# Kernel optimization log

Measured on AMD Instinct MI355X. Metric: run time of the kernel, lower is better.

## Reference

```python
import jax, jax.numpy as jnp
import numpy as np
from jax import lax

EPS = 1e-5
HEADS = 8

def _proj(x, i, w1, b1, g1, be1, m1, v1, w2, b2, g2, be2, m2, v2):
    # Conv2d(1,8,3,1,1) -> BN(8) -> ReLU -> Conv2d(8,1,3,1,1) -> BN(1) -> ReLU (eval-mode BN)
    dn = ('NCHW', 'OIHW', 'NCHW')
    def bn(y, g, b, m, v):
        return g[None, :, None, None] * (y - m[None, :, None, None]) * lax.rsqrt(v + EPS)[None, :, None, None] + b[None, :, None, None]
    y = lax.conv_general_dilated(x, w1[i], (1, 1), 'SAME', dimension_numbers=dn) + b1[i][None, :, None, None]
    y = jax.nn.relu(bn(y, g1[i], be1[i], m1[i], v1[i]))
    y = lax.conv_general_dilated(y, w2[i], (1, 1), 'SAME', dimension_numbers=dn) + b2[i][None, :, None, None]
    return jax.nn.relu(bn(y, g2[i], be2[i], m2[i], v2[i]))

def setup_inputs() -> dict:
    key = jax.random.key(0)
    ks = jax.random.split(key, 4)
    B, L, D = 4, 512, 512
    X = jax.random.normal(ks[0], (B, L, D), dtype=jnp.float32)
    valid_lens = jax.random.randint(ks[1], (B,), 1, L + 1, dtype=jnp.int32)
    # stacked params for the 4 projection blocks: 0=Q, 1=K, 2=V, 3=out
    w1 = jax.random.normal(ks[2], (4, 8, 1, 3, 3), dtype=jnp.float32) * 0.2
    w2 = jax.random.normal(ks[3], (4, 1, 8, 3, 3), dtype=jnp.float32) * 0.2
    b1 = jnp.zeros((4, 8), jnp.float32); b2 = jnp.zeros((4, 1), jnp.float32)
    g1 = jnp.ones((4, 8), jnp.float32);  g2 = jnp.ones((4, 1), jnp.float32)
    be1 = jnp.zeros((4, 8), jnp.float32); be2 = jnp.zeros((4, 1), jnp.float32)
    m1 = jnp.zeros((4, 8), jnp.float32);  m2 = jnp.zeros((4, 1), jnp.float32)
    v1 = jnp.ones((4, 8), jnp.float32);   v2 = jnp.ones((4, 1), jnp.float32)
    return {"X": X, "valid_lens": valid_lens, "w1": w1, "b1": b1, "g1": g1, "be1": be1,
            "m1": m1, "v1": v1, "w2": w2, "b2": b2, "g2": g2, "be2": be2, "m2": m2, "v2": v2}

def reference(X, valid_lens, w1, b1, g1, be1, m1, v1, w2, b2, g2, be2, m2, v2):
    B, L, D = X.shape
    H = HEADS
    d = D // H
    p = (w1, b1, g1, be1, m1, v1, w2, b2, g2, be2, m2, v2)
    X4 = X[:, None]  # [B,1,L,D]
    Q = _proj(X4, 0, *p)
    K = _proj(X4, 1, *p)
    V = _proj(X4, 2, *p)
    def split(Y):  # [B,1,L,D] -> [B,H,L,d]
        return Y.reshape(B, L, H, d).transpose(0, 2, 1, 3)
    q, k, v = split(Q), split(K), split(V)
    # cross-head scores: score[b,i,j,m,n] = <q[b,i,m], k[b,j,n]> / sqrt(d)
    score = jnp.einsum('bimd,bjnd->bijmn', q, k) / jnp.sqrt(jnp.float32(d))
    attn = jax.nn.softmax(score, axis=-1)  # [B,H,H,L,L]
    # context[b,i,m] = sum_j attn[b,i,j] @ v[b,j]  (sum over second head axis)
    ctx = jnp.einsum('bijmn,bjnd->bimd', attn, v)  # [B,H,L,d]
    ctx = ctx.transpose(0, 2, 1, 3).reshape(B, L, D)
    out = _proj(ctx[:, None], 3, *p).reshape(B, L, D)
    return out, attn
```

## Files before the change

kernel.cpp:

```cpp
#include <hip/hip_runtime.h>


__device__ __forceinline__ void fma4(float4& a, float s, const float4& v) {
  a.x = fmaf(s, v.x, a.x);
  a.y = fmaf(s, v.y, a.y);
  a.z = fmaf(s, v.z, a.z);
  a.w = fmaf(s, v.w, a.w);
}

__global__ __launch_bounds__(256)
void conv_proj_kernel(const float* __restrict__ in, int nparts,
                      float* __restrict__ out, int fixed_proj,
                      const float* __restrict__ w1, const float* __restrict__ b1,
                      const float* __restrict__ g1, const float* __restrict__ be1,
                      const float* __restrict__ m1, const float* __restrict__ v1,
                      const float* __restrict__ w2, const float* __restrict__ b2,
                      const float* __restrict__ g2, const float* __restrict__ be2,
                      const float* __restrict__ m2, const float* __restrict__ v2)
{
  __shared__ float xs[36][36];
  __shared__ float ys[8][34][34];
  __shared__ float w1s[8][9];
  __shared__ float w2s[8][9];
  __shared__ float a1s[8], c1s[8];
  __shared__ float a2s[1], c2s[1];

  const int t = threadIdx.x;
  int proj, b;
  if (fixed_proj < 0) { proj = blockIdx.z >> 2; b = blockIdx.z & 3; }
  else                { proj = fixed_proj;      b = blockIdx.z;     }
  const int h0 = blockIdx.y * 32;
  const int w0 = blockIdx.x * 32;

  if (t < 72) {
    w1s[t / 9][t % 9] = w1[proj * 72 + t];
    w2s[t / 9][t % 9] = w2[proj * 72 + t];
  } else if (t < 80) {
    int ch = t - 72;
    float a = g1[proj * 8 + ch] * rsqrtf(v1[proj * 8 + ch] + 1e-5f);
    a1s[ch] = a;
    c1s[ch] = fmaf(a, b1[proj * 8 + ch] - m1[proj * 8 + ch], be1[proj * 8 + ch]);
  } else if (t == 80) {
    float a = g2[proj] * rsqrtf(v2[proj] + 1e-5f);
    a2s[0] = a;
    c2s[0] = fmaf(a, b2[proj] - m2[proj], be2[proj]);
  }

  for (int idx = t; idx < 36 * 36; idx += 256) {
    int r = idx / 36, c = idx - r * 36;
    int hg = h0 - 2 + r, wg = w0 - 2 + c;
    float val = 0.f;
    if (hg >= 0 && hg < 512 && wg >= 0 && wg < 512) {
      int off = b * 262144 + hg * 512 + wg;
      if (nparts == 1) {
        val = in[off];
      } else {
        #pragma unroll
        for (int p = 0; p < 8; ++p) val += in[p * 1048576 + off];
      }
    }
    xs[r][c] = val;
  }
  __syncthreads();

  for (int idx = t; idx < 34 * 34; idx += 256) {
    int r = idx / 34, c = idx - r * 34;
    int hg1 = h0 - 1 + r, wg1 = w0 - 1 + c;
    bool inside = (hg1 >= 0) & (hg1 < 512) & (wg1 >= 0) & (wg1 < 512);
    float x0 = xs[r    ][c], x1 = xs[r    ][c + 1], x2 = xs[r    ][c + 2];
    float x3 = xs[r + 1][c], x4 = xs[r + 1][c + 1], x5 = xs[r + 1][c + 2];
    float x6 = xs[r + 2][c], x7 = xs[r + 2][c + 1], x8 = xs[r + 2][c + 2];
    #pragma unroll
    for (int ch = 0; ch < 8; ++ch) {
      const float* w = w1s[ch];
      float acc = w[0] * x0 + w[1] * x1 + w[2] * x2
                + w[3] * x3 + w[4] * x4 + w[5] * x5
                + w[6] * x6 + w[7] * x7 + w[8] * x8;
      float y = fmaxf(fmaf(acc, a1s[ch], c1s[ch]), 0.f);
      ys[ch][r][c] = inside ? y : 0.f;
    }
  }
  __syncthreads();

  const int r0 = (t >> 4) * 2;
  const int c0 = (t & 15) * 2;
  float o00 = 0.f, o01 = 0.f, o10 = 0.f, o11 = 0.f;
  #pragma unroll
  for (int ch = 0; ch < 8; ++ch) {
    float win[4][4];
    #pragma unroll
    for (int rr = 0; rr < 4; ++rr) {
      float2 p0 = *(const float2*)&ys[ch][r0 + rr][c0];
      float2 p1 = *(const float2*)&ys[ch][r0 + rr][c0 + 2];
      win[rr][0] = p0.x; win[rr][1] = p0.y; win[rr][2] = p1.x; win[rr][3] = p1.y;
    }
    #pragma unroll
    for (int dh = 0; dh < 3; ++dh)
      #pragma unroll
      for (int dw = 0; dw < 3; ++dw) {
        float wgt = w2s[ch][dh * 3 + dw];
        o00 = fmaf(wgt, win[dh    ][dw    ], o00);
        o01 = fmaf(wgt, win[dh    ][dw + 1], o01);
        o10 = fmaf(wgt, win[dh + 1][dw    ], o10);
        o11 = fmaf(wgt, win[dh + 1][dw + 1], o11);
      }
  }
  const float a2 = a2s[0], cc2 = c2s[0];
  float2 row0 = make_float2(fmaxf(fmaf(o00, a2, cc2), 0.f),
                            fmaxf(fmaf(o01, a2, cc2), 0.f));
  float2 row1 = make_float2(fmaxf(fmaf(o10, a2, cc2), 0.f),
                            fmaxf(fmaf(o11, a2, cc2), 0.f));
  const int sel = (fixed_proj < 0) ? proj : 0;
  float* ob = out + sel * 1048576 + b * 262144;
  *(float2*)&ob[(h0 + r0    ) * 512 + (w0 + c0)] = row0;
  *(float2*)&ob[(h0 + r0 + 1) * 512 + (w0 + c0)] = row1;
}

__global__ __launch_bounds__(256)
void attn_score_kernel(const float* __restrict__ Q, const float* __restrict__ K,
                       float* __restrict__ attn)
{
  __shared__ float qs[16][64];
  __shared__ float kt[64][128];
  const int t  = threadIdx.x;
  const int b  = blockIdx.z;
  const int ij = blockIdx.y;
  const int i  = ij >> 3, j = ij & 7;
  const int m0 = blockIdx.x * 16;

  {
    int m = t >> 4, d0 = (t & 15) * 4;
    float4 qv = *(const float4*)&Q[b * 262144 + (m0 + m) * 512 + i * 64 + d0];
    *(float4*)&qs[m][d0] = make_float4(qv.x * 0.125f, qv.y * 0.125f,
                                       qv.z * 0.125f, qv.w * 0.125f);
  }

  const int tm = t >> 5;
  const int tn = t & 31;
  float S[4][8];

  #pragma unroll
  for (int c = 0; c < 4; ++c) {
    __syncthreads();
    {
      int n = t >> 1, d0 = (t & 1) * 32;
      const float* kp = &K[b * 262144 + (c * 128 + n) * 512 + j * 64 + d0];
      #pragma unroll
      for (int q4 = 0; q4 < 8; ++q4) {
        float4 kv = *(const float4*)&kp[q4 * 4];
        kt[d0 + q4 * 4 + 0][n] = kv.x;
        kt[d0 + q4 * 4 + 1][n] = kv.y;
        kt[d0 + q4 * 4 + 2][n] = kv.z;
        kt[d0 + q4 * 4 + 3][n] = kv.w;
      }
    }
    __syncthreads();
    float acc[8] = {0.f, 0.f, 0.f, 0.f, 0.f, 0.f, 0.f, 0.f};
    #pragma unroll 4
    for (int dd = 0; dd < 64; dd += 4) {
      float4 q0 = *(const float4*)&qs[tm    ][dd];
      float4 q1 = *(const float4*)&qs[tm + 8][dd];
      float4 k0 = *(const float4*)&kt[dd    ][tn * 4];
      float4 k1 = *(const float4*)&kt[dd + 1][tn * 4];
      float4 k2 = *(const float4*)&kt[dd + 2][tn * 4];
      float4 k3 = *(const float4*)&kt[dd + 3][tn * 4];
      acc[0] = fmaf(q0.x,k0.x, fmaf(q0.y,k1.x, fmaf(q0.z,k2.x, fmaf(q0.w,k3.x, acc[0]))));
      acc[1] = fmaf(q0.x,k0.y, fmaf(q0.y,k1.y, fmaf(q0.z,k2.y, fmaf(q0.w,k3.y, acc[1]))));
      acc[2] = fmaf(q0.x,k0.z, fmaf(q0.y,k1.z, fmaf(q0.z,k2.z, fmaf(q0.w,k3.z, acc[2]))));
      acc[3] = fmaf(q0.x,k0.w, fmaf(q0.y,k1.w, fmaf(q0.z,k2.w, fmaf(q0.w,k3.w, acc[3]))));
      acc[4] = fmaf(q1.x,k0.x, fmaf(q1.y,k1.x, fmaf(q1.z,k2.x, fmaf(q1.w,k3.x, acc[4]))));
      acc[5] = fmaf(q1.x,k0.y, fmaf(q1.y,k1.y, fmaf(q1.z,k2.y, fmaf(q1.w,k3.y, acc[5]))));
      acc[6] = fmaf(q1.x,k0.z, fmaf(q1.y,k1.z, fmaf(q1.z,k2.z, fmaf(q1.w,k3.z, acc[6]))));
      acc[7] = fmaf(q1.x,k0.w, fmaf(q1.y,k1.w, fmaf(q1.z,k2.w, fmaf(q1.w,k3.w, acc[7]))));
    }
    #pragma unroll
    for (int u = 0; u < 8; ++u) S[c][u] = acc[u];
  }

  float* ap = attn + (size_t)((b * 8 + i) * 8 + j) * 262144;
  #pragma unroll
  for (int mm = 0; mm < 2; ++mm) {
    int m = tm + mm * 8;
    float mx = -3.0e38f;
    #pragma unroll
    for (int c = 0; c < 4; ++c)
      #pragma unroll
      for (int nn = 0; nn < 4; ++nn)
        mx = fmaxf(mx, S[c][mm * 4 + nn]);
    #pragma unroll
    for (int off = 1; off < 32; off <<= 1)
      mx = fmaxf(mx, __shfl_xor(mx, off));
    float sum = 0.f;
    #pragma unroll
    for (int c = 0; c < 4; ++c)
      #pragma unroll
      for (int nn = 0; nn < 4; ++nn) {
        float e = __expf(S[c][mm * 4 + nn] - mx);
        S[c][mm * 4 + nn] = e;
        sum += e;
      }
    #pragma unroll
    for (int off = 1; off < 32; off <<= 1)
      sum += __shfl_xor(sum, off);
    float rinv = 1.0f / sum;
    float* rowp = ap + (size_t)(m0 + m) * 512;
    #pragma unroll
    for (int c = 0; c < 4; ++c) {
      float4 o = make_float4(S[c][mm * 4 + 0] * rinv, S[c][mm * 4 + 1] * rinv,
                             S[c][mm * 4 + 2] * rinv, S[c][mm * 4 + 3] * rinv);
      *(float4*)&rowp[c * 128 + tn * 4] = o;
    }
  }
}

__global__ __launch_bounds__(256)
void ctx_kernel(const float* __restrict__ attn, const float* __restrict__ V,
                float* __restrict__ ctxp)
{
  __shared__ float Pt[32][132];
  __shared__ float Vs[32][64];
  const int t  = threadIdx.x;
  const int m0 = blockIdx.x * 128;
  const int j  = blockIdx.y;
  const int b  = blockIdx.z >> 3;
  const int i  = blockIdx.z & 7;

  const float* ap = attn + (size_t)((b * 8 + i) * 8 + j) * 262144;
  const float* vp = V + b * 262144 + j * 64;

  const int tmg = t >> 4;
  const int td  = t & 15;
  float4 acc[8];
  #pragma unroll
  for (int r = 0; r < 8; ++r) acc[r] = make_float4(0.f, 0.f, 0.f, 0.f);

  for (int c = 0; c < 16; ++c) {
    __syncthreads();
    {
      int m = t >> 1, k0 = (t & 1) * 16;
      const float* pr = ap + (size_t)(m0 + m) * 512 + c * 32 + k0;
      #pragma unroll
      for (int q4 = 0; q4 < 4; ++q4) {
        float4 pv = *(const float4*)&pr[q4 * 4];
        Pt[k0 + q4 * 4 + 0][m] = pv.x;
        Pt[k0 + q4 * 4 + 1][m] = pv.y;
        Pt[k0 + q4 * 4 + 2][m] = pv.z;
        Pt[k0 + q4 * 4 + 3][m] = pv.w;
      }
    }
    #pragma unroll
    for (int u = 0; u < 2; ++u) {
      int idx = t + u * 256;
      int k = idx >> 4, f = idx & 15;
      *(float4*)&Vs[k][f * 4] = *(const float4*)&vp[(size_t)(c * 32 + k) * 512 + f * 4];
    }
    __syncthreads();
    #pragma unroll 8
    for (int k = 0; k < 32; ++k) {
      float4 pa = *(const float4*)&Pt[k][tmg * 8];
      float4 pb = *(const float4*)&Pt[k][tmg * 8 + 4];
      float4 vv = *(const float4*)&Vs[k][td * 4];
      fma4(acc[0], pa.x, vv);
      fma4(acc[1], pa.y, vv);
      fma4(acc[2], pa.z, vv);
      fma4(acc[3], pa.w, vv);
      fma4(acc[4], pb.x, vv);
      fma4(acc[5], pb.y, vv);
      fma4(acc[6], pb.z, vv);
      fma4(acc[7], pb.w, vv);
    }
  }
  float* op = ctxp + j * 1048576 + b * 262144 + i * 64 + td * 4;
  #pragma unroll
  for (int r = 0; r < 8; ++r) {
    *(float4*)&op[(size_t)(m0 + tmg * 8 + r) * 512] = acc[r];
  }
}

extern "C" void kernel_launch(void* const* d_in, const int* in_sizes, int n_in,
                              void* d_out, int out_size, void* d_ws, size_t ws_size,
                              hipStream_t stream)
{
  const float* X   = (const float*)d_in[0];
  const float* w1  = (const float*)d_in[2];
  const float* b1  = (const float*)d_in[3];
  const float* g1  = (const float*)d_in[4];
  const float* be1 = (const float*)d_in[5];
  const float* m1  = (const float*)d_in[6];
  const float* v1  = (const float*)d_in[7];
  const float* w2  = (const float*)d_in[8];
  const float* b2  = (const float*)d_in[9];
  const float* g2  = (const float*)d_in[10];
  const float* be2 = (const float*)d_in[11];
  const float* m2  = (const float*)d_in[12];
  const float* v2  = (const float*)d_in[13];

  float* ws   = (float*)d_ws;
  float* Qb   = ws;
  float* Kb   = ws + 1048576;
  float* Vb   = ws + 2097152;
  float* ctxp = ws + 3145728;
  float* outp = (float*)d_out;
  float* attn = outp + 1048576;

  conv_proj_kernel<<<dim3(16, 16, 12), 256, 0, stream>>>(
      X, 1, ws, -1, w1, b1, g1, be1, m1, v1, w2, b2, g2, be2, m2, v2);

  attn_score_kernel<<<dim3(32, 64, 4), 256, 0, stream>>>(Qb, Kb, attn);

  ctx_kernel<<<dim3(4, 8, 32), 256, 0, stream>>>(attn, Vb, ctxp);

  conv_proj_kernel<<<dim3(16, 16, 4), 256, 0, stream>>>(
      ctxp, 8, outp, 3, w1, b1, g1, be1, m1, v1, w2, b2, g2, be2, m2, v2);
}
```

Before: 581.2 us.

## Fuse attention score softmax with context matmul, reusing probabilities in registers

Merges the score/softmax kernel and the context kernel into one. Each block now covers 32 query rows and keeps the normalized probabilities in registers, staging them through shared memory to multiply with V. This removes the second kernel's re-read of the 64 MB attention tensor. The tile grows to 32 rows, shared-memory rows are padded, and shared memory is reused across phases, which raises register use and may lower occupancy.

```diff
diff --git a/kernel.cpp b/kernel.cpp
--- a/kernel.cpp
+++ b/kernel.cpp
@@ -117,27 +117,37 @@
 }
 
 __global__ __launch_bounds__(256)
-void attn_score_kernel(const float* __restrict__ Q, const float* __restrict__ K,
-                       float* __restrict__ attn)
+void attn_fused_kernel(const float* __restrict__ Q, const float* __restrict__ K,
+                       const float* __restrict__ V,
+                       float* __restrict__ attn, float* __restrict__ ctxp)
 {
-  __shared__ float qs[16][64];
-  __shared__ float kt[64][128];
+  __shared__ __align__(16) float smem[12928];
+  float* qs = smem;
+  float* kt = smem + 2176;
+  float* Pc = smem;
+  float* Vc = smem + 4224;
+
   const int t  = threadIdx.x;
   const int b  = blockIdx.z;
   const int ij = blockIdx.y;
   const int i  = ij >> 3, j = ij & 7;
-  const int m0 = blockIdx.x * 16;
-
-  {
-    int m = t >> 4, d0 = (t & 15) * 4;
-    float4 qv = *(const float4*)&Q[b * 262144 + (m0 + m) * 512 + i * 64 + d0];
-    *(float4*)&qs[m][d0] = make_float4(qv.x * 0.125f, qv.y * 0.125f,
-                                       qv.z * 0.125f, qv.w * 0.125f);
-  }
+  const int m0 = blockIdx.x * 32;
 
   const int tm = t >> 5;
   const int tn = t & 31;
-  float S[4][8];
+
+  {
+    int m = t >> 3, d0 = (t & 7) * 8;
+    const float* qp = &Q[b * 262144 + (m0 + m) * 512 + i * 64 + d0];
+    float4 qa = *(const float4*)qp;
+    float4 qb = *(const float4*)(qp + 4);
+    *(float4*)&qs[m * 68 + d0] =
+        make_float4(qa.x * 0.125f, qa.y * 0.125f, qa.z * 0.125f, qa.w * 0.125f);
+    *(float4*)&qs[m * 68 + d0 + 4] =
+        make_float4(qb.x * 0.125f, qb.y * 0.125f, qb.z * 0.125f, qb.w * 0.125f);
+  }
+
+  float S[4][4][4];
 
   #pragma unroll
   for (int c = 0; c < 4; ++c) {
@@ -148,133 +158,107 @@
       #pragma unroll
       for (int q4 = 0; q4 < 8; ++q4) {
         float4 kv = *(const float4*)&kp[q4 * 4];
-        kt[d0 + q4 * 4 + 0][n] = kv.x;
-        kt[d0 + q4 * 4 + 1][n] = kv.y;
-        kt[d0 + q4 * 4 + 2][n] = kv.z;
-        kt[d0 + q4 * 4 + 3][n] = kv.w;
-      }
-    }
-    __syncthreads();
-    float acc[8] = {0.f, 0.f, 0.f, 0.f, 0.f, 0.f, 0.f, 0.f};
-    #pragma unroll 4
+        kt[(d0 + q4 * 4 + 0) * 132 + n] = kv.x;
+        kt[(d0 + q4 * 4 + 1) * 132 + n] = kv.y;
+        kt[(d0 + q4 * 4 + 2) * 132 + n] = kv.z;
+        kt[(d0 + q4 * 4 + 3) * 132 + n] = kv.w;
+      }
+    }
+    __syncthreads();
+    #pragma unroll
+    for (int mm = 0; mm < 4; ++mm)
+      #pragma unroll
+      for (int nn = 0; nn < 4; ++nn) S[c][mm][nn] = 0.f;
+    #pragma unroll 2
     for (int dd = 0; dd < 64; dd += 4) {
-      float4 q0 = *(const float4*)&qs[tm    ][dd];
-      float4 q1 = *(const float4*)&qs[tm + 8][dd];
-      float4 k0 = *(const float4*)&kt[dd    ][tn * 4];
-      float4 k1 = *(const float4*)&kt[dd + 1][tn * 4];
-      float4 k2 = *(const float4*)&kt[dd + 2][tn * 4];
-      float4 k3 = *(const float4*)&kt[dd + 3][tn * 4];
-      acc[0] = fmaf(q0.x,k0.x, fmaf(q0.y,k1.x, fmaf(q0.z,k2.x, fmaf(q0.w,k3.x, acc[0]))));
-      acc[1] = fmaf(q0.x,k0.y, fmaf(q0.y,k1.y, fmaf(q0.z,k2.y, fmaf(q0.w,k3.y, acc[1]))));
-      acc[2] = fmaf(q0.x,k0.z, fmaf(q0.y,k1.z, fmaf(q0.z,k2.z, fmaf(q0.w,k3.z, acc[2]))));
-      acc[3] = fmaf(q0.x,k0.w, fmaf(q0.y,k1.w, fmaf(q0.z,k2.w, fmaf(q0.w,k3.w, acc[3]))));
-      acc[4] = fmaf(q1.x,k0.x, fmaf(q1.y,k1.x, fmaf(q1.z,k2.x, fmaf(q1.w,k3.x, acc[4]))));
-      acc[5] = fmaf(q1.x,k0.y, fmaf(q1.y,k1.y, fmaf(q1.z,k2.y, fmaf(q1.w,k3.y, acc[5]))));
-      acc[6] = fmaf(q1.x,k0.z, fmaf(q1.y,k1.z, fmaf(q1.z,k2.z, fmaf(q1.w,k3.z, acc[6]))));
-      acc[7] = fmaf(q1.x,k0.w, fmaf(q1.y,k1.w, fmaf(q1.z,k2.w, fmaf(q1.w,k3.w, acc[7]))));
-    }
-    #pragma unroll
-    for (int u = 0; u < 8; ++u) S[c][u] = acc[u];
+      float4 k0 = *(const float4*)&kt[(dd + 0) * 132 + tn * 4];
+      float4 k1 = *(const float4*)&kt[(dd + 1) * 132 + tn * 4];
+      float4 k2 = *(const float4*)&kt[(dd + 2) * 132 + tn * 4];
+      float4 k3 = *(const float4*)&kt[(dd + 3) * 132 + tn * 4];
+      #pragma unroll
+      for (int mm = 0; mm < 4; ++mm) {
+        float4 qv = *(const float4*)&qs[(tm + 8 * mm) * 68 + dd];
+        S[c][mm][0] = fmaf(qv.x, k0.x, fmaf(qv.y, k1.x, fmaf(qv.z, k2.x, fmaf(qv.w, k3.x, S[c][mm][0]))));
+        S[c][mm][1] = fmaf(qv.x, k0.y, fmaf(qv.y, k1.y, fmaf(qv.z, k2.y, fmaf(qv.w, k3.y, S[c][mm][1]))));
+        S[c][mm][2] = fmaf(qv.x, k0.z, fmaf(qv.y, k1.z, fmaf(qv.z, k2.z, fmaf(qv.w, k3.z, S[c][mm][2]))));
+        S[c][mm][3] = fmaf(qv.x, k0.w, fmaf(qv.y, k1.w, fmaf(qv.z, k2.w, fmaf(qv.w, k3.w, S[c][mm][3]))));
+      }
+    }
   }
 
   float* ap = attn + (size_t)((b * 8 + i) * 8 + j) * 262144;
   #pragma unroll
-  for (int mm = 0; mm < 2; ++mm) {
-    int m = tm + mm * 8;
+  for (int mm = 0; mm < 4; ++mm) {
     float mx = -3.0e38f;
     #pragma unroll
     for (int c = 0; c < 4; ++c)
       #pragma unroll
-      for (int nn = 0; nn < 4; ++nn)
-        mx = fmaxf(mx, S[c][mm * 4 + nn]);
-    #pragma unroll
-    for (int off = 1; off < 32; off <<= 1)
-      mx = fmaxf(mx, __shfl_xor(mx, off));
+      for (int nn = 0; nn < 4; ++nn) mx = fmaxf(mx, S[c][mm][nn]);
+    #pragma unroll
+    for (int off = 1; off < 32; off <<= 1) mx = fmaxf(mx, __shfl_xor(mx, off));
     float sum = 0.f;
     #pragma unroll
     for (int c = 0; c < 4; ++c)
       #pragma unroll
       for (int nn = 0; nn < 4; ++nn) {
-        float e = __expf(S[c][mm * 4 + nn] - mx);
-        S[c][mm * 4 + nn] = e;
+        float e = __expf(S[c][mm][nn] - mx);
+        S[c][mm][nn] = e;
         sum += e;
       }
     #pragma unroll
-    for (int off = 1; off < 32; off <<= 1)
-      sum += __shfl_xor(sum, off);
+    for (int off = 1; off < 32; off <<= 1) sum += __shfl_xor(sum, off);
     float rinv = 1.0f / sum;
-    float* rowp = ap + (size_t)(m0 + m) * 512;
+    float* rowp = ap + (size_t)(m0 + tm + 8 * mm) * 512;
     #pragma unroll
     for (int c = 0; c < 4; ++c) {
-      float4 o = make_float4(S[c][mm * 4 + 0] * rinv, S[c][mm * 4 + 1] * rinv,
-                             S[c][mm * 4 + 2] * rinv, S[c][mm * 4 + 3] * rinv);
+      float4 o = make_float4(S[c][mm][0] * rinv, S[c][mm][1] * rinv,
+                             S[c][mm][2] * rinv, S[c][mm][3] * rinv);
+      S[c][mm][0] = o.x; S[c][mm][1] = o.y; S[c][mm][2] = o.z; S[c][mm][3] = o.w;
       *(float4*)&rowp[c * 128 + tn * 4] = o;
     }
   }
-}
-
-__global__ __launch_bounds__(256)
-void ctx_kernel(const float* __restrict__ attn, const float* __restrict__ V,
-                float* __restrict__ ctxp)
-{
-  __shared__ float Pt[32][132];
-  __shared__ float Vs[32][64];
-  const int t  = threadIdx.x;
-  const int m0 = blockIdx.x * 128;
-  const int j  = blockIdx.y;
-  const int b  = blockIdx.z >> 3;
-  const int i  = blockIdx.z & 7;
-
-  const float* ap = attn + (size_t)((b * 8 + i) * 8 + j) * 262144;
+
+  const int rp = t >> 4;
+  const int cd = (t & 15) * 4;
+  float4 acc0 = make_float4(0.f, 0.f, 0.f, 0.f);
+  float4 acc1 = make_float4(0.f, 0.f, 0.f, 0.f);
   const float* vp = V + b * 262144 + j * 64;
 
-  const int tmg = t >> 4;
-  const int td  = t & 15;
-  float4 acc[8];
-  #pragma unroll
-  for (int r = 0; r < 8; ++r) acc[r] = make_float4(0.f, 0.f, 0.f, 0.f);
-
-  for (int c = 0; c < 16; ++c) {
-    __syncthreads();
+  #pragma unroll
+  for (int c = 0; c < 4; ++c) {
+    __syncthreads();
+    #pragma unroll
+    for (int mm = 0; mm < 4; ++mm) {
+      *(float4*)&Pc[(tm + 8 * mm) * 132 + tn * 4] =
+          make_float4(S[c][mm][0], S[c][mm][1], S[c][mm][2], S[c][mm][3]);
+    }
     {
-      int m = t >> 1, k0 = (t & 1) * 16;
-      const float* pr = ap + (size_t)(m0 + m) * 512 + c * 32 + k0;
-      #pragma unroll
-      for (int q4 = 0; q4 < 4; ++q4) {
-        float4 pv = *(const float4*)&pr[q4 * 4];
-        Pt[k0 + q4 * 4 + 0][m] = pv.x;
-        Pt[k0 + q4 * 4 + 1][m] = pv.y;
-        Pt[k0 + q4 * 4 + 2][m] = pv.z;
-        Pt[k0 + q4 * 4 + 3][m] = pv.w;
-      }
-    }
-    #pragma unroll
-    for (int u = 0; u < 2; ++u) {
-      int idx = t + u * 256;
-      int k = idx >> 4, f = idx & 15;
-      *(float4*)&Vs[k][f * 4] = *(const float4*)&vp[(size_t)(c * 32 + k) * 512 + f * 4];
-    }
-    __syncthreads();
-    #pragma unroll 8
-    for (int k = 0; k < 32; ++k) {
-      float4 pa = *(const float4*)&Pt[k][tmg * 8];
-      float4 pb = *(const float4*)&Pt[k][tmg * 8 + 4];
-      float4 vv = *(const float4*)&Vs[k][td * 4];
-      fma4(acc[0], pa.x, vv);
-      fma4(acc[1], pa.y, vv);
-      fma4(acc[2], pa.z, vv);
-      fma4(acc[3], pa.w, vv);
-      fma4(acc[4], pb.x, vv);
-      fma4(acc[5], pb.y, vv);
-      fma4(acc[6], pb.z, vv);
-      fma4(acc[7], pb.w, vv);
-    }
-  }
-  float* op = ctxp + j * 1048576 + b * 262144 + i * 64 + td * 4;
-  #pragma unroll
-  for (int r = 0; r < 8; ++r) {
-    *(float4*)&op[(size_t)(m0 + tmg * 8 + r) * 512] = acc[r];
-  }
+      int k0 = t >> 4, d0 = (t & 15) * 4;
+      #pragma unroll
+      for (int q8 = 0; q8 < 8; ++q8) {
+        int k = k0 + q8 * 16;
+        *(float4*)&Vc[k * 68 + d0] =
+            *(const float4*)&vp[(size_t)(c * 128 + k) * 512 + d0];
+      }
+    }
+    __syncthreads();
+    #pragma unroll 2
+    for (int k = 0; k < 128; k += 4) {
+      float4 pa = *(const float4*)&Pc[rp * 132 + k];
+      float4 pb = *(const float4*)&Pc[(rp + 16) * 132 + k];
+      float4 v0 = *(const float4*)&Vc[(k + 0) * 68 + cd];
+      float4 v1 = *(const float4*)&Vc[(k + 1) * 68 + cd];
+      float4 v2 = *(const float4*)&Vc[(k + 2) * 68 + cd];
+      float4 v3 = *(const float4*)&Vc[(k + 3) * 68 + cd];
+      fma4(acc0, pa.x, v0); fma4(acc0, pa.y, v1);
+      fma4(acc0, pa.z, v2); fma4(acc0, pa.w, v3);
+      fma4(acc1, pb.x, v0); fma4(acc1, pb.y, v1);
+      fma4(acc1, pb.z, v2); fma4(acc1, pb.w, v3);
+    }
+  }
+  float* op = ctxp + j * 1048576 + b * 262144 + i * 64 + cd;
+  *(float4*)&op[(size_t)(m0 + rp)      * 512] = acc0;
+  *(float4*)&op[(size_t)(m0 + rp + 16) * 512] = acc1;
 }
 
 extern "C" void kernel_launch(void* const* d_in, const int* in_sizes, int n_in,
@@ -306,9 +290,7 @@
   conv_proj_kernel<<<dim3(16, 16, 12), 256, 0, stream>>>(
       X, 1, ws, -1, w1, b1, g1, be1, m1, v1, w2, b2, g2, be2, m2, v2);
 
-  attn_score_kernel<<<dim3(32, 64, 4), 256, 0, stream>>>(Qb, Kb, attn);
-
-  ctx_kernel<<<dim3(4, 8, 32), 256, 0, stream>>>(attn, Vb, ctxp);
+  attn_fused_kernel<<<dim3(16, 64, 4), 256, 0, stream>>>(Qb, Kb, Vb, attn, ctxp);
 
   conv_proj_kernel<<<dim3(16, 16, 4), 256, 0, stream>>>(
       ctxp, 8, outp, 3, w1, b1, g1, be1, m1, v1, w2, b2, g2, be2, m2, v2);
```

After: 555.1 us. -4.5%, faster.
